# Performance work log

Hardware: AMD Instinct MI355X
Metric: run time of the kernel (lower is better)

Reference implementation:

```python
import jax, jax.numpy as jnp
import numpy as np

B, N, PHY, C, HID, FC, L, E = 2, 8192, 2, 64, 64, 128, 3, 524288

def _ln(x, g, b, eps=1e-5):
    mu = jnp.mean(x, axis=-1, keepdims=True)
    var = jnp.mean((x - mu) ** 2, axis=-1, keepdims=True)
    return (x - mu) * jax.lax.rsqrt(var + eps) * g + b

def setup_inputs() -> dict:
    key = jax.random.key(0)
    ks = jax.random.split(key, 24)
    s = 1.0 / np.sqrt(C)
    inp = {
        'x': jax.random.normal(ks[0], (B, N, 5), jnp.float32),
        'edge_index': jax.random.randint(ks[1], (2, E), 0, B * N, jnp.int32),
        'fc0_w': jax.random.normal(ks[2], (C, 4), jnp.float32) * 0.5,
        'fc0_b': jnp.zeros((C,), jnp.float32),
        'ln0_g': jnp.ones((C,), jnp.float32),
        'ln0_b': jnp.zeros((C,), jnp.float32),
        'gg_fc1_w': jax.random.normal(ks[3], (L, HID, C), jnp.float32) * s,
        'gg_fc1_b': jnp.zeros((L, HID), jnp.float32),
        'gg_fc2_w': jax.random.normal(ks[4], (L, C, HID), jnp.float32) * s,
        'gg_fc2_b': jnp.zeros((L, C), jnp.float32),
        'gg_weight': jax.random.uniform(ks[5], (L, HID), jnp.float32) + 0.5,
        'gg_freq': jax.random.normal(ks[6], (L, PHY, HID), jnp.float32) * (2 * np.pi),
        'wc_w': jax.random.normal(ks[7], (L, C, C), jnp.float32) * s,
        'wc_b': jnp.zeros((L, C), jnp.float32),
        'ln_g': jnp.ones((L, C), jnp.float32),
        'ln_b': jnp.zeros((L, C), jnp.float32),
        'fc1_w': jax.random.normal(ks[8], (FC, C), jnp.float32) * s,
        'fc1_b': jnp.zeros((FC,), jnp.float32),
        'fc2_w': jax.random.normal(ks[9], (1, FC), jnp.float32) / np.sqrt(FC),
        'fc2_b': jnp.zeros((1,), jnp.float32),
    }
    return inp

def reference(x, edge_index, fc0_w, fc0_b, ln0_g, ln0_b, gg_fc1_w, gg_fc1_b,
              gg_fc2_w, gg_fc2_b, gg_weight, gg_freq, wc_w, wc_b, ln_g, ln_b,
              fc1_w, fc1_b, fc2_w, fc2_b):
    grid = x[:, :, 2:4]           # (B,N,PHY): columns in_dim-phy_dim .. -1
    gw = x[:, :, 4]               # (B,N) grid_weight
    feat = x[:, :, :4]            # (B,N,in_dim)
    src, dst = edge_index[0], edge_index[1]
    grid_f = grid.reshape(-1, PHY)
    gw_f = gw.reshape(-1)
    vec = grid_f[src] - grid_f[dst]                      # (E,PHY)
    dist2 = jnp.sum(vec * vec, axis=-1, keepdims=True)   # (E,1)
    wgt_src = gw_f[src][:, None]                          # (E,1)

    h = feat @ fc0_w.T + fc0_b                            # (B,N,C)
    h = _ln(h, ln0_g, ln0_b)
    for l in range(L):
        w = gg_weight[l]                                  # (HID,)
        gauss = jnp.sqrt((w / jnp.pi) ** PHY) * jnp.exp(-w * dist2)  # (E,HID)
        fourier = jnp.sin(vec @ gg_freq[l])               # (E,HID)
        morlet = gauss * fourier
        hl = h @ gg_fc1_w[l].T + gg_fc1_b[l]              # (B,N,HID)
        val = morlet * hl.reshape(-1, HID)[src] * wgt_src # (E,HID)
        agg = jax.ops.segment_sum(val, dst, num_segments=B * N)
        x1 = agg.reshape(B, N, HID) @ gg_fc2_w[l].T + gg_fc2_b[l]
        x2 = h @ wc_w[l].T + wc_b[l]                      # pointwise Conv1d
        h = _ln(x1 + x2, ln_g[l], ln_b[l])
        if l != L - 1:
            h = jax.nn.gelu(h, approximate=False)
    h = jax.nn.gelu(h @ fc1_w.T + fc1_b, approximate=False)
    return h @ fc2_w.T + fc2_b                            # (B,N,1)
```

## Files before the change

### kernel.cpp

```cpp
#include <hip/hip_runtime.h>
#include <hip/hip_bf16.h>

#define M_NODES 16384
#define E_EDGES 524288
#define ASTR 68

typedef short short8 __attribute__((ext_vector_type(8)));
typedef float f32x4 __attribute__((ext_vector_type(4)));
typedef unsigned int uint4v __attribute__((ext_vector_type(4)));

#define PK_W1 0
#define PK_WC 12288
#define PK_W2 24576
#define PK_FC1 36864
#define PK_TOTAL 45056

static __device__ __forceinline__ float wredsum(float v) {
#pragma unroll
  for (int o = 32; o > 0; o >>= 1) v += __shfl_xor(v, o, 64);
  return v;
}

static __device__ __forceinline__ float gelu_exact(float x) {
  return 0.5f * x * (1.0f + erff(x * 0.70710678118654752440f));
}

static __device__ __forceinline__ unsigned int bsplit(float x) {
  unsigned int u = __float_as_uint(x);
  unsigned int hb = (u + 0x7FFFu + ((u >> 16) & 1u)) >> 16;
  float hf = __uint_as_float(hb << 16);
  float r = x - hf;
  unsigned int v = __float_as_uint(r);
  unsigned int lb = (v + 0x7FFFu + ((v >> 16) & 1u)) >> 16;
  return (hb & 0xFFFFu) | (lb << 16);
}

struct Frag { short8 hi, lo; };

static __device__ __forceinline__ Frag load_afrag(const unsigned int* a) {
  uint4v u0 = *(const uint4v*)a;
  uint4v u1 = *(const uint4v*)(a + 4);
  Frag f;
#pragma unroll
  for (int j = 0; j < 4; ++j) {
    f.hi[j]     = (short)(u0[j] & 0xFFFFu);
    f.lo[j]     = (short)(u0[j] >> 16);
    f.hi[j + 4] = (short)(u1[j] & 0xFFFFu);
    f.lo[j + 4] = (short)(u1[j] >> 16);
  }
  return f;
}

static __device__ __forceinline__ Frag load_bfrag(const float* __restrict__ w) {
  float4 w0 = *(const float4*)w;
  float4 w1 = *(const float4*)(w + 4);
  float v[8] = {w0.x, w0.y, w0.z, w0.w, w1.x, w1.y, w1.z, w1.w};
  Frag f;
#pragma unroll
  for (int j = 0; j < 8; ++j) {
    unsigned int p = bsplit(v[j]);
    f.hi[j] = (short)(p & 0xFFFFu);
    f.lo[j] = (short)(p >> 16);
  }
  return f;
}

static __device__ __forceinline__ f32x4 mfma3(const Frag& a, const Frag& b, f32x4 c) {
  c = __builtin_amdgcn_mfma_f32_16x16x32_bf16(a.hi, b.hi, c, 0, 0, 0);
  c = __builtin_amdgcn_mfma_f32_16x16x32_bf16(a.lo, b.hi, c, 0, 0, 0);
  c = __builtin_amdgcn_mfma_f32_16x16x32_bf16(a.hi, b.lo, c, 0, 0, 0);
  return c;
}

static __device__ __forceinline__ Frag load_bpk(const short* __restrict__ P, int S, int n, int off) {
  Frag f;
  f.hi = *(const short8*)(P + n * 64 + off);
  f.lo = *(const short8*)(P + S + n * 64 + off);
  return f;
}

static __device__ __forceinline__ f32x4 gemm16p(const unsigned int* __restrict__ A,
                                                const short* __restrict__ P, int S,
                                                int n, int c, int q) {
  Frag a0 = load_afrag(A + c * ASTR + 8 * q);
  Frag a1 = load_afrag(A + c * ASTR + 32 + 8 * q);
  Frag b0 = load_bpk(P, S, n, 8 * q);
  Frag b1 = load_bpk(P, S, n, 32 + 8 * q);
  f32x4 acc = {0.f, 0.f, 0.f, 0.f};
  acc = mfma3(a0, b0, acc);
  acc = mfma3(a1, b1, acc);
  return acc;
}

__global__ __launch_bounds__(256) void k_front(
    const float* __restrict__ x,
    const float* __restrict__ fc0_w, const float* __restrict__ fc0_b,
    const float* __restrict__ ln0_g, const float* __restrict__ ln0_b,
    const float* __restrict__ gg_fc1_w, const float* __restrict__ gg_fc1_b,
    const float* __restrict__ wc_w, const float* __restrict__ wc_b,
    const float* __restrict__ gg_fc2_w, const float* __restrict__ fc1_w,
    const int* __restrict__ ei, int* __restrict__ cnt, short* __restrict__ pk,
    float2* __restrict__ grid2, float* __restrict__ gwf,
    float* __restrict__ hl, float* __restrict__ x2T)
{
  __shared__ unsigned int A[16 * ASTR];
  const int bid = blockIdx.x;
  const int tid = threadIdx.x;

  if (bid >= 3072) {
    int i = (bid - 3072) * 256 + tid;
    float v = (i < PK_WC)  ? gg_fc1_w[i]
            : (i < PK_W2)  ? wc_w[i - PK_WC]
            : (i < PK_FC1) ? gg_fc2_w[i - PK_W2]
                           : fc1_w[i - PK_FC1];
    int mb, sz;
    if (i < PK_FC1) { mb = i & ~4095; sz = 4096; } else { mb = PK_FC1; sz = 8192; }
    int k = i - mb;
    unsigned int p = bsplit(v);
    pk[2 * mb + k]      = (short)(p & 0xFFFFu);
    pk[2 * mb + sz + k] = (short)(p >> 16);
    return;
  }
  if (bid >= 1024) {
    int e = (bid - 1024) * 256 + tid;
    atomicAdd(&cnt[ei[E_EDGES + e]], 1);
    return;
  }

  const int lane = tid & 63, w = tid >> 6;
  const int tilebase = bid * 16;

  float fw0 = fc0_w[lane * 4 + 0], fw1 = fc0_w[lane * 4 + 1];
  float fw2v = fc0_w[lane * 4 + 2], fw3 = fc0_w[lane * 4 + 3];
  float fb = fc0_b[lane], g0 = ln0_g[lane], bb0 = ln0_b[lane];

#pragma unroll
  for (int i = 0; i < 4; ++i) {
    int node = tilebase + 4 * w + i;
    float xv0 = x[node * 5 + 0], xv1 = x[node * 5 + 1], xv2 = x[node * 5 + 2];
    float xv3 = x[node * 5 + 3], xv4 = x[node * 5 + 4];
    float acc = fb + xv0 * fw0 + xv1 * fw1 + xv2 * fw2v + xv3 * fw3;
    float mean = wredsum(acc) * (1.0f / 64.0f);
    float d = acc - mean;
    float var = wredsum(d * d) * (1.0f / 64.0f);
    float hv = d * rsqrtf(var + 1e-5f) * g0 + bb0;
    A[(4 * w + i) * ASTR + lane] = bsplit(hv);
    if (lane == 0) { grid2[node] = make_float2(xv2, xv3); gwf[node] = xv4; }
  }
  __syncthreads();

  const int c = lane & 15, q = lane >> 4;
  const int n = 16 * w + c;

  {
    Frag a0 = load_afrag(A + c * ASTR + 8 * q);
    Frag a1 = load_afrag(A + c * ASTR + 32 + 8 * q);
    Frag b0 = load_bfrag(gg_fc1_w + n * 64 + 8 * q);
    Frag b1 = load_bfrag(gg_fc1_w + n * 64 + 32 + 8 * q);
    f32x4 acc = {0.f, 0.f, 0.f, 0.f};
    acc = mfma3(a0, b0, acc);
    acc = mfma3(a1, b1, acc);
    float b1v = gg_fc1_b[n];
#pragma unroll
    for (int r = 0; r < 4; ++r)
      hl[(tilebase + 4 * q + r) * 64 + n] = acc[r] + b1v;

    Frag c0 = load_bfrag(wc_w + n * 64 + 8 * q);
    Frag c1 = load_bfrag(wc_w + n * 64 + 32 + 8 * q);
    f32x4 ac2 = {0.f, 0.f, 0.f, 0.f};
    ac2 = mfma3(a0, c0, ac2);
    ac2 = mfma3(a1, c1, ac2);
    float wcbv = wc_b[n];
    *(float4*)(x2T + n * M_NODES + tilebase + 4 * q) =
        make_float4(ac2[0] + wcbv, ac2[1] + wcbv, ac2[2] + wcbv, ac2[3] + wcbv);
  }
}

__global__ __launch_bounds__(1024) void k_scan(const int* __restrict__ cnt,
                                               int* __restrict__ row_start,
                                               int* __restrict__ cursor)
{
  const int PER = M_NODES / 1024;
  const int t = threadIdx.x;
  const int base = t * PER;
  int local[PER];
  int s = 0;
#pragma unroll
  for (int k = 0; k < PER; ++k) { local[k] = cnt[base + k]; s += local[k]; }

  __shared__ int part[1024];
  part[t] = s;
  __syncthreads();
  for (int off = 1; off < 1024; off <<= 1) {
    int v = (t >= off) ? part[t - off] : 0;
    __syncthreads();
    part[t] += v;
    __syncthreads();
  }
  int run = part[t] - s;
#pragma unroll
  for (int k = 0; k < PER; ++k) {
    row_start[base + k] = run;
    cursor[base + k] = run;
    run += local[k];
  }
  if (t == 1023) row_start[M_NODES] = run;
}

__global__ __launch_bounds__(256) void k_scatter(
    const int* __restrict__ ei, const float2* __restrict__ grid2,
    const float* __restrict__ gwf, int* __restrict__ cursor,
    float4* __restrict__ rec)
{
  int e = blockIdx.x * 256 + threadIdx.x;
  if (e < E_EDGES) {
    int s = ei[e];
    int dd = ei[E_EDGES + e];
    int pos = atomicAdd(&cursor[dd], 1);
    float2 gs = grid2[s], gd = grid2[dd];
    rec[pos] = make_float4(gs.x - gd.x, gs.y - gd.y, gwf[s], __int_as_float(s));
  }
}

__global__ __launch_bounds__(256) void k_agg(
    const float4* __restrict__ rec, const int* __restrict__ row_start,
    const float* __restrict__ hl,
    const float* __restrict__ gw, const float* __restrict__ freq,
    unsigned int* __restrict__ aggp)
{
  __shared__ float4 LR[4][64];
  const int lane = threadIdx.x & 63;
  const int w = threadIdx.x >> 6;
  const int node = blockIdx.x * 4 + w;

  const float wv = gw[lane];
  const float nwl2 = -wv * 1.44269504088896340736f;
  const float lc = log2f(wv * 0.31830988618379067154f);
  const float f0s = freq[lane] * 0.15915494309189533577f;
  const float f1s = freq[64 + lane] * 0.15915494309189533577f;

  const int beg = row_start[node];
  const int end = row_start[node + 1];
  const float* hlp = hl + lane;
  float4* LRw = LR[w];

  float acc = 0.0f;

  for (int base = beg; base < end; base += 64) {
    const int cn = min(64, end - base);
    if (lane < cn) LRw[lane] = rec[base + lane];

    float4 RA[8], RB[8];
    float HA[8], HB[8];

    auto ldg = [&](float4* R, float* H, int off) {
#pragma unroll
      for (int u = 0; u < 8; ++u) {
        int j = off + u; j = (j < cn) ? j : (cn - 1);
        R[u] = LRw[j];
      }
#pragma unroll
      for (int u = 0; u < 8; ++u)
        H[u] = hlp[__float_as_int(R[u].w) * 64];
    };
    auto cmp8 = [&](const float4* R, const float* H, int off) {
#pragma unroll
      for (int u = 0; u < 8; ++u) {
        if (off + u < cn) {
          float dist2 = __builtin_fmaf(R[u].x, R[u].x, R[u].y * R[u].y);
          float gs = __builtin_amdgcn_exp2f(__builtin_fmaf(nwl2, dist2, lc));
          float rev = __builtin_fmaf(R[u].x, f0s, R[u].y * f1s);
          float fo = __builtin_amdgcn_sinf(__builtin_amdgcn_fractf(rev));
          acc = __builtin_fmaf(gs * fo * H[u], R[u].z, acc);
        }
      }
    };

    const int Gp = (cn + 7) >> 3;
    ldg(RA, HA, 0);
    int g = 0;
    for (; g + 2 < Gp; g += 2) {
      ldg(RB, HB, 8 * (g + 1));
      cmp8(RA, HA, 8 * g);
      ldg(RA, HA, 8 * (g + 2));
      cmp8(RB, HB, 8 * (g + 1));
    }
    if (g + 1 < Gp) {
      ldg(RB, HB, 8 * (g + 1));
      cmp8(RA, HA, 8 * g);
      cmp8(RB, HB, 8 * (g + 1));
    } else {
      cmp8(RA, HA, 8 * g);
    }
  }
  aggp[node * 64 + lane] = bsplit(acc);
}

__global__ __launch_bounds__(256) void k_post_mid(
    const unsigned int* __restrict__ aggp,
    const short* __restrict__ pw2, const float* __restrict__ b2,
    const float* __restrict__ lng, const float* __restrict__ lnb,
    const short* __restrict__ pnw1, const float* __restrict__ nb1,
    const short* __restrict__ pnwc, const float* __restrict__ nwcb,
    float* __restrict__ hl, float* __restrict__ x2T)
{
  __shared__ unsigned int A[16 * ASTR];
  __shared__ float PS[4][16], PQ[4][16];
  const int tid = threadIdx.x, lane = tid & 63, w = tid >> 6;
  const int tilebase = blockIdx.x * 16;
  const int c = lane & 15, q = lane >> 4;
  const int n = 16 * w + c;

  float4 x2v = *(const float4*)(x2T + n * M_NODES + tilebase + 4 * q);
  float lg = lng[n], lb = lnb[n], vb = b2[n];
  float b1v = nb1[n], wcbv = nwcb[n];
  Frag wb0 = load_bpk(pw2, 4096, n, 8 * q);
  Frag wb1 = load_bpk(pw2, 4096, n, 32 + 8 * q);

  {
    int i = tid * 4;
    *(uint4v*)(A + (i >> 6) * ASTR + (i & 63)) = *(const uint4v*)(aggp + tilebase * 64 + i);
  }
  __syncthreads();

  Frag a0 = load_afrag(A + c * ASTR + 8 * q);
  Frag a1 = load_afrag(A + c * ASTR + 32 + 8 * q);
  f32x4 acc = {0.f, 0.f, 0.f, 0.f};
  acc = mfma3(a0, wb0, acc);
  acc = mfma3(a1, wb1, acc);

  float S[4];
#pragma unroll
  for (int r = 0; r < 4; ++r) S[r] = acc[r] + vb + x2v[r];

#pragma unroll
  for (int r = 0; r < 4; ++r) {
    float s1 = S[r], s2 = S[r] * S[r];
#pragma unroll
    for (int m = 1; m < 16; m <<= 1) {
      s1 += __shfl_xor(s1, m, 64);
      s2 += __shfl_xor(s2, m, 64);
    }
    if (c == 0) { PS[w][4 * q + r] = s1; PQ[w][4 * q + r] = s2; }
  }
  __syncthreads();

#pragma unroll
  for (int r = 0; r < 4; ++r) {
    int row = 4 * q + r;
    float sum = PS[0][row] + PS[1][row] + PS[2][row] + PS[3][row];
    float sq  = PQ[0][row] + PQ[1][row] + PQ[2][row] + PQ[3][row];
    float mean = sum * (1.0f / 64.0f);
    float var = sq * (1.0f / 64.0f) - mean * mean;
    float hv = (S[r] - mean) * rsqrtf(var + 1e-5f) * lg + lb;
    hv = gelu_exact(hv);
    A[row * ASTR + n] = bsplit(hv);
  }
  __syncthreads();

  f32x4 h1 = gemm16p(A, pnw1, 4096, n, c, q);
#pragma unroll
  for (int r = 0; r < 4; ++r)
    hl[(tilebase + 4 * q + r) * 64 + n] = h1[r] + b1v;

  f32x4 hx = gemm16p(A, pnwc, 4096, n, c, q);
  *(float4*)(x2T + n * M_NODES + tilebase + 4 * q) =
      make_float4(hx[0] + wcbv, hx[1] + wcbv, hx[2] + wcbv, hx[3] + wcbv);
}

__global__ __launch_bounds__(256) void k_post_last(
    const unsigned int* __restrict__ aggp,
    const short* __restrict__ pw2, const float* __restrict__ b2,
    const float* __restrict__ lng, const float* __restrict__ lnb,
    const float* __restrict__ x2T,
    const short* __restrict__ pfc1, const float* __restrict__ fc1b,
    const float* __restrict__ fw2, const float* __restrict__ fb2,
    float* __restrict__ out)
{
  __shared__ unsigned int A[16 * ASTR];
  __shared__ float PS[4][16], PQ[4][16];
  const int tid = threadIdx.x, lane = tid & 63, w = tid >> 6;
  const int tilebase = blockIdx.x * 16;
  const int c = lane & 15, q = lane >> 4;
  const int n = 16 * w + c;

  float4 x2v = *(const float4*)(x2T + n * M_NODES + tilebase + 4 * q);
  float lg = lng[n], lb = lnb[n], vb = b2[n];
  Frag wb0 = load_bpk(pw2, 4096, n, 8 * q);
  Frag wb1 = load_bpk(pw2, 4096, n, 32 + 8 * q);

  {
    int i = tid * 4;
    *(uint4v*)(A + (i >> 6) * ASTR + (i & 63)) = *(const uint4v*)(aggp + tilebase * 64 + i);
  }
  __syncthreads();

  Frag a0 = load_afrag(A + c * ASTR + 8 * q);
  Frag a1 = load_afrag(A + c * ASTR + 32 + 8 * q);
  f32x4 acc = {0.f, 0.f, 0.f, 0.f};
  acc = mfma3(a0, wb0, acc);
  acc = mfma3(a1, wb1, acc);

  float S[4];
#pragma unroll
  for (int r = 0; r < 4; ++r) S[r] = acc[r] + vb + x2v[r];

#pragma unroll
  for (int r = 0; r < 4; ++r) {
    float s1 = S[r], s2 = S[r] * S[r];
#pragma unroll
    for (int m = 1; m < 16; m <<= 1) {
      s1 += __shfl_xor(s1, m, 64);
      s2 += __shfl_xor(s2, m, 64);
    }
    if (c == 0) { PS[w][4 * q + r] = s1; PQ[w][4 * q + r] = s2; }
  }
  __syncthreads();

#pragma unroll
  for (int r = 0; r < 4; ++r) {
    int row = 4 * q + r;
    float sum = PS[0][row] + PS[1][row] + PS[2][row] + PS[3][row];
    float sq  = PQ[0][row] + PQ[1][row] + PQ[2][row] + PQ[3][row];
    float mean = sum * (1.0f / 64.0f);
    float var = sq * (1.0f / 64.0f) - mean * mean;
    float hv = (S[r] - mean) * rsqrtf(var + 1e-5f) * lg + lb;
    A[row * ASTR + n] = bsplit(hv);
  }
  __syncthreads();

  Frag ha0 = load_afrag(A + c * ASTR + 8 * q);
  Frag ha1 = load_afrag(A + c * ASTR + 32 + 8 * q);
  float p[4] = {0.f, 0.f, 0.f, 0.f};
#pragma unroll
  for (int half = 0; half < 2; ++half) {
    int row = 32 * w + 16 * half + c;
    Frag b0 = load_bpk(pfc1, 8192, row, 8 * q);
    Frag b1 = load_bpk(pfc1, 8192, row, 32 + 8 * q);
    f32x4 a = {0.f, 0.f, 0.f, 0.f};
    a = mfma3(ha0, b0, a);
    a = mfma3(ha1, b1, a);
    float fbv = fc1b[row], fwv = fw2[row];
#pragma unroll
    for (int r = 0; r < 4; ++r) p[r] += gelu_exact(a[r] + fbv) * fwv;
  }
#pragma unroll
  for (int r = 0; r < 4; ++r) {
    float s = p[r];
#pragma unroll
    for (int m = 1; m < 16; m <<= 1) s += __shfl_xor(s, m, 64);
    if (c == 0) PS[w][4 * q + r] = s;
  }
  __syncthreads();
  if (tid < 16)
    out[tilebase + tid] = PS[0][tid] + PS[1][tid] + PS[2][tid] + PS[3][tid] + fb2[0];
}

extern "C" void kernel_launch(void* const* d_in, const int* in_sizes, int n_in,
                              void* d_out, int out_size, void* d_ws, size_t ws_size,
                              hipStream_t stream) {
  const float* x     = (const float*)d_in[0];
  const int* ei      = (const int*)d_in[1];
  const float* fc0_w = (const float*)d_in[2];
  const float* fc0_b = (const float*)d_in[3];
  const float* ln0_g = (const float*)d_in[4];
  const float* ln0_b = (const float*)d_in[5];
  const float* gg_fc1_w = (const float*)d_in[6];
  const float* gg_fc1_b = (const float*)d_in[7];
  const float* gg_fc2_w = (const float*)d_in[8];
  const float* gg_fc2_b = (const float*)d_in[9];
  const float* gg_weight = (const float*)d_in[10];
  const float* gg_freq   = (const float*)d_in[11];
  const float* wc_w = (const float*)d_in[12];
  const float* wc_b = (const float*)d_in[13];
  const float* ln_g = (const float*)d_in[14];
  const float* ln_b = (const float*)d_in[15];
  const float* fc1_w = (const float*)d_in[16];
  const float* fc1_b = (const float*)d_in[17];
  const float* fc2_w = (const float*)d_in[18];
  const float* fc2_b = (const float*)d_in[19];

  char* ws = (char*)d_ws;
  size_t off = 0;
  auto alloc = [&](size_t bytes) -> void* {
    void* p = ws + off;
    off = (off + bytes + 255) & ~(size_t)255;
    return p;
  };
  float2* grid2 = (float2*)alloc((size_t)M_NODES * 8);
  float*  gwf   = (float*)alloc((size_t)M_NODES * 4);
  float*  hl    = (float*)alloc((size_t)M_NODES * 64 * 4);
  unsigned int* aggp = (unsigned int*)alloc((size_t)M_NODES * 64 * 4);
  float*  x2T   = (float*)alloc((size_t)M_NODES * 64 * 4);
  int*    cnt   = (int*)alloc((size_t)M_NODES * 4);
  int*    cursor= (int*)alloc((size_t)M_NODES * 4);
  int*    row_st= (int*)alloc((size_t)(M_NODES + 1) * 4);
  float4* rec   = (float4*)alloc((size_t)E_EDGES * 16);
  short*  pk    = (short*)alloc((size_t)PK_TOTAL * 2 * 2);
  (void)ws_size; (void)in_sizes; (void)n_in; (void)out_size;

  hipMemsetAsync(cnt, 0, (size_t)M_NODES * 4, stream);

  k_front<<<3248, 256, 0, stream>>>(x, fc0_w, fc0_b, ln0_g, ln0_b,
                                    gg_fc1_w, gg_fc1_b, wc_w, wc_b,
                                    gg_fc2_w, fc1_w,
                                    ei, cnt, pk, grid2, gwf, hl, x2T);
  k_scan<<<1, 1024, 0, stream>>>(cnt, row_st, cursor);
  k_scatter<<<E_EDGES / 256, 256, 0, stream>>>(ei, grid2, gwf, cursor, rec);

  for (int l = 0; l < 3; ++l) {
    k_agg<<<M_NODES / 4, 256, 0, stream>>>(rec, row_st, hl,
                                           gg_weight + l * 64, gg_freq + l * 128, aggp);
    const short* pw2 = pk + 2 * (PK_W2 + l * 4096);
    if (l < 2) {
      k_post_mid<<<M_NODES / 16, 256, 0, stream>>>(
          aggp, pw2, gg_fc2_b + l * 64,
          ln_g + l * 64, ln_b + l * 64,
          pk + 2 * (PK_W1 + (l + 1) * 4096), gg_fc1_b + (l + 1) * 64,
          pk + 2 * (PK_WC + (l + 1) * 4096), wc_b + (l + 1) * 64,
          hl, x2T);
    } else {
      k_post_last<<<M_NODES / 16, 256, 0, stream>>>(
          aggp, pw2, gg_fc2_b + l * 64,
          ln_g + l * 64, ln_b + l * 64,
          x2T,
          pk + 2 * PK_FC1, fc1_b, fc2_w, fc2_b,
          (float*)d_out);
    }
  }
}
```

Before: 260.5 us.

## Fuse edge aggregation into per-layer post kernels with ping-pong hl buffers

Merges the per-node edge aggregation kernel into the following MFMA/LayerNorm post kernel, so each 16-node block first aggregates its nodes' edges directly into shared memory and then applies fc2, LN, and the next layer's projections. This removes the aggp round-trip through global memory and halves the number of per-layer launches. hl is double-buffered because other blocks still read the previous layer's hl while this layer writes the new one. The edge loop now reads rec directly instead of staging it in LDS, and each wave processes 4 nodes serially, giving fewer blocks (1024 instead of 4096) and potentially less latency hiding on the gather-heavy phase.

```diff
diff --git a/kernel.cpp b/kernel.cpp
--- a/kernel.cpp
+++ b/kernel.cpp
@@ -77,19 +77,6 @@
   f.hi = *(const short8*)(P + n * 64 + off);
   f.lo = *(const short8*)(P + S + n * 64 + off);
   return f;
-}
-
-static __device__ __forceinline__ f32x4 gemm16p(const unsigned int* __restrict__ A,
-                                                const short* __restrict__ P, int S,
-                                                int n, int c, int q) {
-  Frag a0 = load_afrag(A + c * ASTR + 8 * q);
-  Frag a1 = load_afrag(A + c * ASTR + 32 + 8 * q);
-  Frag b0 = load_bpk(P, S, n, 8 * q);
-  Frag b1 = load_bpk(P, S, n, 32 + 8 * q);
-  f32x4 acc = {0.f, 0.f, 0.f, 0.f};
-  acc = mfma3(a0, b0, acc);
-  acc = mfma3(a1, b1, acc);
-  return acc;
 }
 
 __global__ __launch_bounds__(256) void k_front(
@@ -222,87 +209,71 @@
   }
 }
 
-__global__ __launch_bounds__(256) void k_agg(
+#define EDGE_PHASE()                                                          \
+  const float wv = gw[lane];                                                  \
+  const float nwl2 = -wv * 1.44269504088896340736f;                           \
+  const float lc = log2f(wv * 0.31830988618379067154f);                       \
+  const float f0s = freq[lane] * 0.15915494309189533577f;                     \
+  const float f1s = freq[64 + lane] * 0.15915494309189533577f;                \
+  const float* hlp = hl_in + lane;                                            \
+  for (int nn = 0; nn < 4; ++nn) {                                            \
+    const int node = tilebase + 4 * w + nn;                                   \
+    const int beg = row_start[node];                                          \
+    const int cn = row_start[node + 1] - beg;                                 \
+    float acc = 0.f;                                                          \
+    if (cn > 0) {                                                             \
+      float4 RA[8], RB[8]; float HA[8], HB[8];                                \
+      auto ldg = [&](float4* R, float* H, int off) {                          \
+        _Pragma("unroll")                                                     \
+        for (int u = 0; u < 8; ++u) {                                         \
+          int j = off + u; j = (j < cn) ? j : (cn - 1);                       \
+          R[u] = rec[beg + j];                                                \
+        }                                                                     \
+        _Pragma("unroll")                                                     \
+        for (int u = 0; u < 8; ++u)                                           \
+          H[u] = hlp[__float_as_int(R[u].w) * 64];                            \
+      };                                                                      \
+      auto cmp8 = [&](const float4* R, const float* H, int off) {             \
+        _Pragma("unroll")                                                     \
+        for (int u = 0; u < 8; ++u) {                                         \
+          if (off + u < cn) {                                                 \
+            float dist2 = __builtin_fmaf(R[u].x, R[u].x, R[u].y * R[u].y);    \
+            float gs = __builtin_amdgcn_exp2f(__builtin_fmaf(nwl2, dist2, lc));\
+            float rev = __builtin_fmaf(R[u].x, f0s, R[u].y * f1s);            \
+            float fo = __builtin_amdgcn_sinf(__builtin_amdgcn_fractf(rev));   \
+            acc = __builtin_fmaf(gs * fo * H[u], R[u].z, acc);                \
+          }                                                                   \
+        }                                                                     \
+      };                                                                      \
+      const int Gp = (cn + 7) >> 3;                                           \
+      ldg(RA, HA, 0);                                                         \
+      int g = 0;                                                              \
+      for (; g + 2 < Gp; g += 2) {                                            \
+        ldg(RB, HB, 8 * (g + 1));                                             \
+        cmp8(RA, HA, 8 * g);                                                  \
+        ldg(RA, HA, 8 * (g + 2));                                             \
+        cmp8(RB, HB, 8 * (g + 1));                                            \
+      }                                                                       \
+      if (g + 1 < Gp) {                                                       \
+        ldg(RB, HB, 8 * (g + 1));                                             \
+        cmp8(RA, HA, 8 * g);                                                  \
+        cmp8(RB, HB, 8 * (g + 1));                                            \
+      } else {                                                                \
+        cmp8(RA, HA, 8 * g);                                                  \
+      }                                                                       \
+    }                                                                         \
+    A[(4 * w + nn) * ASTR + lane] = bsplit(acc);                              \
+  }
+
+__global__ __launch_bounds__(256) void k_layer_mid(
     const float4* __restrict__ rec, const int* __restrict__ row_start,
-    const float* __restrict__ hl,
+    const float* __restrict__ hl_in,
     const float* __restrict__ gw, const float* __restrict__ freq,
-    unsigned int* __restrict__ aggp)
-{
-  __shared__ float4 LR[4][64];
-  const int lane = threadIdx.x & 63;
-  const int w = threadIdx.x >> 6;
-  const int node = blockIdx.x * 4 + w;
-
-  const float wv = gw[lane];
-  const float nwl2 = -wv * 1.44269504088896340736f;
-  const float lc = log2f(wv * 0.31830988618379067154f);
-  const float f0s = freq[lane] * 0.15915494309189533577f;
-  const float f1s = freq[64 + lane] * 0.15915494309189533577f;
-
-  const int beg = row_start[node];
-  const int end = row_start[node + 1];
-  const float* hlp = hl + lane;
-  float4* LRw = LR[w];
-
-  float acc = 0.0f;
-
-  for (int base = beg; base < end; base += 64) {
-    const int cn = min(64, end - base);
-    if (lane < cn) LRw[lane] = rec[base + lane];
-
-    float4 RA[8], RB[8];
-    float HA[8], HB[8];
-
-    auto ldg = [&](float4* R, float* H, int off) {
-#pragma unroll
-      for (int u = 0; u < 8; ++u) {
-        int j = off + u; j = (j < cn) ? j : (cn - 1);
-        R[u] = LRw[j];
-      }
-#pragma unroll
-      for (int u = 0; u < 8; ++u)
-        H[u] = hlp[__float_as_int(R[u].w) * 64];
-    };
-    auto cmp8 = [&](const float4* R, const float* H, int off) {
-#pragma unroll
-      for (int u = 0; u < 8; ++u) {
-        if (off + u < cn) {
-          float dist2 = __builtin_fmaf(R[u].x, R[u].x, R[u].y * R[u].y);
-          float gs = __builtin_amdgcn_exp2f(__builtin_fmaf(nwl2, dist2, lc));
-          float rev = __builtin_fmaf(R[u].x, f0s, R[u].y * f1s);
-          float fo = __builtin_amdgcn_sinf(__builtin_amdgcn_fractf(rev));
-          acc = __builtin_fmaf(gs * fo * H[u], R[u].z, acc);
-        }
-      }
-    };
-
-    const int Gp = (cn + 7) >> 3;
-    ldg(RA, HA, 0);
-    int g = 0;
-    for (; g + 2 < Gp; g += 2) {
-      ldg(RB, HB, 8 * (g + 1));
-      cmp8(RA, HA, 8 * g);
-      ldg(RA, HA, 8 * (g + 2));
-      cmp8(RB, HB, 8 * (g + 1));
-    }
-    if (g + 1 < Gp) {
-      ldg(RB, HB, 8 * (g + 1));
-      cmp8(RA, HA, 8 * g);
-      cmp8(RB, HB, 8 * (g + 1));
-    } else {
-      cmp8(RA, HA, 8 * g);
-    }
-  }
-  aggp[node * 64 + lane] = bsplit(acc);
-}
-
-__global__ __launch_bounds__(256) void k_post_mid(
-    const unsigned int* __restrict__ aggp,
     const short* __restrict__ pw2, const float* __restrict__ b2,
     const float* __restrict__ lng, const float* __restrict__ lnb,
     const short* __restrict__ pnw1, const float* __restrict__ nb1,
     const short* __restrict__ pnwc, const float* __restrict__ nwcb,
-    float* __restrict__ hl, float* __restrict__ x2T)
+    float* __restrict__ hl_out, float* __restrict__ x2T)
 {
   __shared__ unsigned int A[16 * ASTR];
   __shared__ float PS[4][16], PQ[4][16];
@@ -314,13 +285,15 @@
   float4 x2v = *(const float4*)(x2T + n * M_NODES + tilebase + 4 * q);
   float lg = lng[n], lb = lnb[n], vb = b2[n];
   float b1v = nb1[n], wcbv = nwcb[n];
+
+  EDGE_PHASE()
+
   Frag wb0 = load_bpk(pw2, 4096, n, 8 * q);
   Frag wb1 = load_bpk(pw2, 4096, n, 32 + 8 * q);
-
-  {
-    int i = tid * 4;
-    *(uint4v*)(A + (i >> 6) * ASTR + (i & 63)) = *(const uint4v*)(aggp + tilebase * 64 + i);
-  }
+  Frag n10 = load_bpk(pnw1, 4096, n, 8 * q);
+  Frag n11 = load_bpk(pnw1, 4096, n, 32 + 8 * q);
+  Frag nc0 = load_bpk(pnwc, 4096, n, 8 * q);
+  Frag nc1 = load_bpk(pnwc, 4096, n, 32 + 8 * q);
   __syncthreads();
 
   Frag a0 = load_afrag(A + c * ASTR + 8 * q);
@@ -358,18 +331,27 @@
   }
   __syncthreads();
 
-  f32x4 h1 = gemm16p(A, pnw1, 4096, n, c, q);
+  Frag h0 = load_afrag(A + c * ASTR + 8 * q);
+  Frag h1 = load_afrag(A + c * ASTR + 32 + 8 * q);
+
+  f32x4 hh = {0.f, 0.f, 0.f, 0.f};
+  hh = mfma3(h0, n10, hh);
+  hh = mfma3(h1, n11, hh);
 #pragma unroll
   for (int r = 0; r < 4; ++r)
-    hl[(tilebase + 4 * q + r) * 64 + n] = h1[r] + b1v;
-
-  f32x4 hx = gemm16p(A, pnwc, 4096, n, c, q);
+    hl_out[(tilebase + 4 * q + r) * 64 + n] = hh[r] + b1v;
+
+  f32x4 hx = {0.f, 0.f, 0.f, 0.f};
+  hx = mfma3(h0, nc0, hx);
+  hx = mfma3(h1, nc1, hx);
   *(float4*)(x2T + n * M_NODES + tilebase + 4 * q) =
       make_float4(hx[0] + wcbv, hx[1] + wcbv, hx[2] + wcbv, hx[3] + wcbv);
 }
 
-__global__ __launch_bounds__(256) void k_post_last(
-    const unsigned int* __restrict__ aggp,
+__global__ __launch_bounds__(256) void k_layer_last(
+    const float4* __restrict__ rec, const int* __restrict__ row_start,
+    const float* __restrict__ hl_in,
+    const float* __restrict__ gw, const float* __restrict__ freq,
     const short* __restrict__ pw2, const float* __restrict__ b2,
     const float* __restrict__ lng, const float* __restrict__ lnb,
     const float* __restrict__ x2T,
@@ -386,13 +368,11 @@
 
   float4 x2v = *(const float4*)(x2T + n * M_NODES + tilebase + 4 * q);
   float lg = lng[n], lb = lnb[n], vb = b2[n];
+
+  EDGE_PHASE()
+
   Frag wb0 = load_bpk(pw2, 4096, n, 8 * q);
   Frag wb1 = load_bpk(pw2, 4096, n, 32 + 8 * q);
-
-  {
-    int i = tid * 4;
-    *(uint4v*)(A + (i >> 6) * ASTR + (i & 63)) = *(const uint4v*)(aggp + tilebase * 64 + i);
-  }
   __syncthreads();
 
   Frag a0 = load_afrag(A + c * ASTR + 8 * q);
@@ -489,8 +469,8 @@
   };
   float2* grid2 = (float2*)alloc((size_t)M_NODES * 8);
   float*  gwf   = (float*)alloc((size_t)M_NODES * 4);
-  float*  hl    = (float*)alloc((size_t)M_NODES * 64 * 4);
-  unsigned int* aggp = (unsigned int*)alloc((size_t)M_NODES * 64 * 4);
+  float*  hl_a  = (float*)alloc((size_t)M_NODES * 64 * 4);
+  float*  hl_b  = (float*)alloc((size_t)M_NODES * 64 * 4);
   float*  x2T   = (float*)alloc((size_t)M_NODES * 64 * 4);
   int*    cnt   = (int*)alloc((size_t)M_NODES * 4);
   int*    cursor= (int*)alloc((size_t)M_NODES * 4);
@@ -504,28 +484,29 @@
   k_front<<<3248, 256, 0, stream>>>(x, fc0_w, fc0_b, ln0_g, ln0_b,
                                     gg_fc1_w, gg_fc1_b, wc_w, wc_b,
                                     gg_fc2_w, fc1_w,
-                                    ei, cnt, pk, grid2, gwf, hl, x2T);
+                                    ei, cnt, pk, grid2, gwf, hl_a, x2T);
   k_scan<<<1, 1024, 0, stream>>>(cnt, row_st, cursor);
   k_scatter<<<E_EDGES / 256, 256, 0, stream>>>(ei, grid2, gwf, cursor, rec);
 
-  for (int l = 0; l < 3; ++l) {
-    k_agg<<<M_NODES / 4, 256, 0, stream>>>(rec, row_st, hl,
-                                           gg_weight + l * 64, gg_freq + l * 128, aggp);
-    const short* pw2 = pk + 2 * (PK_W2 + l * 4096);
-    if (l < 2) {
-      k_post_mid<<<M_NODES / 16, 256, 0, stream>>>(
-          aggp, pw2, gg_fc2_b + l * 64,
-          ln_g + l * 64, ln_b + l * 64,
-          pk + 2 * (PK_W1 + (l + 1) * 4096), gg_fc1_b + (l + 1) * 64,
-          pk + 2 * (PK_WC + (l + 1) * 4096), wc_b + (l + 1) * 64,
-          hl, x2T);
-    } else {
-      k_post_last<<<M_NODES / 16, 256, 0, stream>>>(
-          aggp, pw2, gg_fc2_b + l * 64,
-          ln_g + l * 64, ln_b + l * 64,
-          x2T,
-          pk + 2 * PK_FC1, fc1_b, fc2_w, fc2_b,
-          (float*)d_out);
-    }
-  }
-}
+  k_layer_mid<<<M_NODES / 16, 256, 0, stream>>>(
+      rec, row_st, hl_a, gg_weight + 0 * 64, gg_freq + 0 * 128,
+      pk + 2 * (PK_W2 + 0 * 4096), gg_fc2_b + 0 * 64,
+      ln_g + 0 * 64, ln_b + 0 * 64,
+      pk + 2 * (PK_W1 + 1 * 4096), gg_fc1_b + 1 * 64,
+      pk + 2 * (PK_WC + 1 * 4096), wc_b + 1 * 64,
+      hl_b, x2T);
+  k_layer_mid<<<M_NODES / 16, 256, 0, stream>>>(
+      rec, row_st, hl_b, gg_weight + 1 * 64, gg_freq + 1 * 128,
+      pk + 2 * (PK_W2 + 1 * 4096), gg_fc2_b + 1 * 64,
+      ln_g + 1 * 64, ln_b + 1 * 64,
+      pk + 2 * (PK_W1 + 2 * 4096), gg_fc1_b + 2 * 64,
+      pk + 2 * (PK_WC + 2 * 4096), wc_b + 2 * 64,
+      hl_a, x2T);
+  k_layer_last<<<M_NODES / 16, 256, 0, stream>>>(
+      rec, row_st, hl_a, gg_weight + 2 * 64, gg_freq + 2 * 128,
+      pk + 2 * (PK_W2 + 2 * 4096), gg_fc2_b + 2 * 64,
+      ln_g + 2 * 64, ln_b + 2 * 64,
+      x2T,
+      pk + 2 * PK_FC1, fc1_b, fc2_w, fc2_b,
+      (float*)d_out);
+}
```

New measurement: 263.5 us. Within noise of the previous version (+1.2%).
